# Kernel optimization log

Measured on AMD Instinct MI355X. Metric: run time of the kernel, lower is better.

Reference implementation:

```python
import jax, jax.numpy as jnp
import numpy as np

C = 1.0  # Poincare ball curvature
EPS = 1e-15


def setup_inputs() -> dict:
    key = jax.random.key(0)
    k1, k2, k3 = jax.random.split(key, 3)
    B, S, D_IN, D_OUT = 16, 8192, 128, 128
    # points strictly inside the unit ball: ||x|| ~ 0.05*sqrt(128) ~ 0.57
    x = 0.05 * jax.random.normal(k1, (B, S, D_IN), dtype=jnp.float32)
    z = 0.01 * jax.random.normal(k2, (D_IN, D_OUT), dtype=jnp.float32)  # init_std=0.01 normal
    r = 0.01 * jax.random.normal(k3, (D_OUT,), dtype=jnp.float32)
    return {"x": x, "z": z, "r": r}


def reference(x, z, r):
    # Poincare MLR (Shimizu et al., Hyperbolic NN++), as in hypll PoincareBall.mlr
    c = jnp.asarray(C, x.dtype)
    cs = jnp.sqrt(c)
    prefix = x.shape[:-1]
    x2 = x.reshape(-1, x.shape[-1])                       # [N, d_in]
    # conformal factor lambda_x = 2 / (1 - c ||x||^2)
    lam = 2.0 / (1.0 - c * jnp.sum(x2 * x2, axis=-1, keepdims=True))  # [N, 1]
    z_norm = jnp.maximum(jnp.linalg.norm(z, axis=0), EPS)             # [d_out]
    two_csr = 2.0 * cs * r                                            # [d_out]
    inner = x2 @ z                                                    # [N, d_out]
    arg = (cs * lam * inner / z_norm) * jnp.cosh(two_csr) - (lam - 1.0) * jnp.sinh(two_csr)
    out = (2.0 * z_norm / cs) * jnp.arcsinh(arg)                      # [N, d_out]
    return out.reshape(*prefix, z.shape[1])
```

## Files before the change

kernel.cpp:

```cpp
#include <hip/hip_runtime.h>
#include <cstdint>


typedef __attribute__((ext_vector_type(8))) short short8;
typedef __attribute__((ext_vector_type(4))) float floatx4;

#define D 128

__device__ inline unsigned bf16_rne(float f) {
    unsigned u = __float_as_uint(f);
    return ((u + 0x7FFFu + ((u >> 16) & 1u)) >> 16) & 0xFFFFu;
}

__global__ void hmlr_prep(const float* __restrict__ z, const float* __restrict__ r,
                          unsigned short* __restrict__ zt, float4* __restrict__ abs4) {
    int n = blockIdx.x;
    int k = threadIdx.x;
    float v = z[k * D + n];
    zt[n * D + k] = (unsigned short)bf16_rne(v);
    float p = v * v;
    #pragma unroll
    for (int off = 32; off >= 1; off >>= 1) p += __shfl_down(p, off, 64);
    __shared__ float tmp[2];
    if ((k & 63) == 0) tmp[k >> 6] = p;
    __syncthreads();
    if (k == 0) {
        float ss = tmp[0] + tmp[1];
        float zn = fmaxf(sqrtf(ss), 1e-15f);
        float tc = 2.0f * r[n];
        abs4[n] = make_float4(coshf(tc) / zn, sinhf(tc), 2.0f * zn, 0.0f);
    }
}

__global__ __launch_bounds__(512, 4) void hmlr_main(const float* __restrict__ x,
                                                    const unsigned short* __restrict__ zt,
                                                    const float4* __restrict__ abs4,
                                                    float* __restrict__ out) {
    __shared__ __align__(16) unsigned char lds[65536];
    #define LDS_Z 32768

    const int t    = threadIdx.x;
    const int w    = t >> 6;
    const int l    = t & 63;
    const int quad = l >> 4;
    const int l15  = l & 15;
    const int l7   = l15 & 7;

    const int rowbase = blockIdx.x * 128 + w * 16;

    const uint4* ztg = reinterpret_cast<const uint4*>(zt);
    uint4 zreg[4];
    #pragma unroll
    for (int i = 0; i < 4; ++i) zreg[i] = ztg[t + (i << 9)];

    const float4* xg = reinterpret_cast<const float4*>(x) + (size_t)blockIdx.x * 4096 + w * 512;
    float4 xv[8];
    #pragma unroll
    for (int j = 0; j < 8; ++j) xv[j] = xg[(j << 6) + l];

    float s[8];
    #pragma unroll
    for (int j = 0; j < 8; ++j) {
        float4 v = xv[j];
        int f   = (j << 6) + l;
        int row = w * 16 + (f >> 5);
        int fc  = f & 31;
        float p = v.x * v.x + v.y * v.y + v.z * v.z + v.w * v.w;
        p += __shfl_xor(p, 1);
        p += __shfl_xor(p, 2);
        p += __shfl_xor(p, 4);
        p += __shfl_xor(p, 8);
        p += __shfl_xor(p, 16);
        s[j] = p;
        unsigned lo = bf16_rne(v.x) | (bf16_rne(v.y) << 16);
        unsigned hi = bf16_rne(v.z) | (bf16_rne(v.w) << 16);
        int byte = (row << 8) + ((((fc >> 1) ^ (row & 7)) << 4)) + ((fc & 1) << 3);
        *reinterpret_cast<uint2*>(&lds[byte]) = make_uint2(lo, hi);
    }

    int idx3 = (l >> 1) & 7;
    float a0 = (idx3 & 1) ? s[1] : s[0];
    float a1 = (idx3 & 1) ? s[3] : s[2];
    float a2 = (idx3 & 1) ? s[5] : s[4];
    float a3 = (idx3 & 1) ? s[7] : s[6];
    float b0 = (idx3 & 2) ? a1 : a0;
    float b1 = (idx3 & 2) ? a3 : a2;
    float vsel = (idx3 & 4) ? b1 : b0;
    float usel = __shfl_xor(vsel, 32);
    float rq = (((l >> 5) & 1) == (l & 1)) ? vsel : usel;

    short8 afrag[4];
    #pragma unroll
    for (int kc = 0; kc < 4; ++kc) {
        int byte = ((w * 16 + l15) << 8) + (((quad + (kc << 2)) ^ l7) << 4);
        afrag[kc] = *reinterpret_cast<const short8*>(&lds[byte]);
    }

    #pragma unroll
    for (int i = 0; i < 4; ++i) {
        int idx = t + (i << 9);
        int row = idx >> 4, c = idx & 15;
        int byte = LDS_Z + (row << 8) + (((c ^ (row & 7)) << 4));
        *reinterpret_cast<uint4*>(&lds[byte]) = zreg[i];
    }
    __syncthreads();

    float4 cst[8];
    #pragma unroll
    for (int nt = 0; nt < 8; ++nt) cst[nt] = abs4[nt * 16 + l15];

    floatx4 acc[8];
    #pragma unroll
    for (int nt = 0; nt < 8; ++nt) acc[nt] = (floatx4){0.f, 0.f, 0.f, 0.f};

    #pragma unroll
    for (int kc = 0; kc < 4; ++kc) {
        #pragma unroll
        for (int nt = 0; nt < 8; ++nt) {
            int byte = LDS_Z + ((nt * 16 + l15) << 8) + (((quad + (kc << 2)) ^ l7) << 4);
            short8 b = *reinterpret_cast<const short8*>(&lds[byte]);
            acc[nt] = __builtin_amdgcn_mfma_f32_16x16x32_bf16(afrag[kc], b, acc[nt], 0, 0, 0);
        }
    }

    #pragma unroll
    for (int reg = 0; reg < 4; ++reg) {
        float rss = __shfl(rq, (quad << 2) | reg);
        float lam = 2.0f / (1.0f - rss);
        float lm1 = lam - 1.0f;
        float* orow = out + (size_t)(rowbase + (quad << 2) + reg) * D + l15;
        #pragma unroll
        for (int nt = 0; nt < 8; ++nt) {
            float inner = acc[nt][reg];
            float arg = __fmaf_rn(lam * inner, cst[nt].x, -lm1 * cst[nt].y);
            float a   = fabsf(arg);
            float as  = __logf(a + __fsqrt_rn(__fmaf_rn(a, a, 1.0f)));
            orow[nt * 16] = copysignf(as, arg) * cst[nt].z;
        }
    }
    #undef LDS_Z
}

extern "C" void kernel_launch(void* const* d_in, const int* in_sizes, int n_in,
                              void* d_out, int out_size, void* d_ws, size_t ws_size,
                              hipStream_t stream) {
    const float* x = (const float*)d_in[0];
    const float* z = (const float*)d_in[1];
    const float* r = (const float*)d_in[2];
    float* out = (float*)d_out;

    char* wsb = (char*)d_ws;
    unsigned short* zt = (unsigned short*)wsb;
    float4* abs4 = (float4*)(wsb + 128 * D * sizeof(unsigned short));

    hmlr_prep<<<128, 128, 0, stream>>>(z, r, zt, abs4);

    const int n_rows = in_sizes[0] / D;
    hmlr_main<<<n_rows / 128, 512, 0, stream>>>(x, zt, abs4, out);
}
```

Before: 125.4 us.

## Stage accumulators through LDS for float4 output stores, compute norms via MFMA

Computes the squared row norms with an extra MFMA of each A fragment against itself, taking the diagonal, in place of the shuffle reductions on the fp32 inputs. The epilogue writes accumulators into reused LDS in two passes and reads them back so each lane stores contiguous float4 rows, giving coalesced output writes. Per-column constants move to separate arrays loaded as float4. The norm is now taken from bf16-rounded inputs, which loses some precision, and the LDS round trip adds traffic and branching.

```diff
diff --git a/kernel.cpp b/kernel.cpp
--- a/kernel.cpp
+++ b/kernel.cpp
@@ -13,7 +13,8 @@
 }
 
 __global__ void hmlr_prep(const float* __restrict__ z, const float* __restrict__ r,
-                          unsigned short* __restrict__ zt, float4* __restrict__ abs4) {
+                          unsigned short* __restrict__ zt, float* __restrict__ An,
+                          float* __restrict__ Bn, float* __restrict__ Sn) {
     int n = blockIdx.x;
     int k = threadIdx.x;
     float v = z[k * D + n];
@@ -28,13 +29,17 @@
         float ss = tmp[0] + tmp[1];
         float zn = fmaxf(sqrtf(ss), 1e-15f);
         float tc = 2.0f * r[n];
-        abs4[n] = make_float4(coshf(tc) / zn, sinhf(tc), 2.0f * zn, 0.0f);
+        An[n] = coshf(tc) / zn;
+        Bn[n] = sinhf(tc);
+        Sn[n] = 2.0f * zn;
     }
 }
 
 __global__ __launch_bounds__(512, 4) void hmlr_main(const float* __restrict__ x,
                                                     const unsigned short* __restrict__ zt,
-                                                    const float4* __restrict__ abs4,
+                                                    const float* __restrict__ An,
+                                                    const float* __restrict__ Bn,
+                                                    const float* __restrict__ Sn,
                                                     float* __restrict__ out) {
     __shared__ __align__(16) unsigned char lds[65536];
     #define LDS_Z 32768
@@ -58,36 +63,17 @@
     #pragma unroll
     for (int j = 0; j < 8; ++j) xv[j] = xg[(j << 6) + l];
 
-    float s[8];
     #pragma unroll
     for (int j = 0; j < 8; ++j) {
         float4 v = xv[j];
         int f   = (j << 6) + l;
         int row = w * 16 + (f >> 5);
         int fc  = f & 31;
-        float p = v.x * v.x + v.y * v.y + v.z * v.z + v.w * v.w;
-        p += __shfl_xor(p, 1);
-        p += __shfl_xor(p, 2);
-        p += __shfl_xor(p, 4);
-        p += __shfl_xor(p, 8);
-        p += __shfl_xor(p, 16);
-        s[j] = p;
         unsigned lo = bf16_rne(v.x) | (bf16_rne(v.y) << 16);
         unsigned hi = bf16_rne(v.z) | (bf16_rne(v.w) << 16);
         int byte = (row << 8) + ((((fc >> 1) ^ (row & 7)) << 4)) + ((fc & 1) << 3);
         *reinterpret_cast<uint2*>(&lds[byte]) = make_uint2(lo, hi);
     }
-
-    int idx3 = (l >> 1) & 7;
-    float a0 = (idx3 & 1) ? s[1] : s[0];
-    float a1 = (idx3 & 1) ? s[3] : s[2];
-    float a2 = (idx3 & 1) ? s[5] : s[4];
-    float a3 = (idx3 & 1) ? s[7] : s[6];
-    float b0 = (idx3 & 2) ? a1 : a0;
-    float b1 = (idx3 & 2) ? a3 : a2;
-    float vsel = (idx3 & 4) ? b1 : b0;
-    float usel = __shfl_xor(vsel, 32);
-    float rq = (((l >> 5) & 1) == (l & 1)) ? vsel : usel;
 
     short8 afrag[4];
     #pragma unroll
@@ -105,16 +91,19 @@
     }
     __syncthreads();
 
-    float4 cst[8];
-    #pragma unroll
-    for (int nt = 0; nt < 8; ++nt) cst[nt] = abs4[nt * 16 + l15];
+    const int col0 = (l & 31) << 2;
+    float4 A4 = *reinterpret_cast<const float4*>(An + col0);
+    float4 B4 = *reinterpret_cast<const float4*>(Bn + col0);
+    float4 S4 = *reinterpret_cast<const float4*>(Sn + col0);
 
     floatx4 acc[8];
     #pragma unroll
     for (int nt = 0; nt < 8; ++nt) acc[nt] = (floatx4){0.f, 0.f, 0.f, 0.f};
+    floatx4 accd = (floatx4){0.f, 0.f, 0.f, 0.f};
 
     #pragma unroll
     for (int kc = 0; kc < 4; ++kc) {
+        accd = __builtin_amdgcn_mfma_f32_16x16x32_bf16(afrag[kc], afrag[kc], accd, 0, 0, 0);
         #pragma unroll
         for (int nt = 0; nt < 8; ++nt) {
             int byte = LDS_Z + ((nt * 16 + l15) << 8) + (((quad + (kc << 2)) ^ l7) << 4);
@@ -123,19 +112,54 @@
         }
     }
 
+    float cand = accd[l15 & 3];
+
+    float4* outv = reinterpret_cast<float4*>(out + (size_t)rowbase * D);
+    const int pbase = w << 12;
+
     #pragma unroll
-    for (int reg = 0; reg < 4; ++reg) {
-        float rss = __shfl(rq, (quad << 2) | reg);
-        float lam = 2.0f / (1.0f - rss);
-        float lm1 = lam - 1.0f;
-        float* orow = out + (size_t)(rowbase + (quad << 2) + reg) * D + l15;
+    for (int pass = 0; pass < 2; ++pass) {
+        if ((quad >> 1) == pass) {
+            int pr = (quad & 1) << 2;
+            #pragma unroll
+            for (int reg = 0; reg < 4; ++reg) {
+                #pragma unroll
+                for (int nt = 0; nt < 8; ++nt) {
+                    int byte = pbase + ((pr + reg) << 9) + ((l15 + (nt << 4)) << 2);
+                    *reinterpret_cast<float*>(&lds[byte]) = acc[nt][reg];
+                }
+            }
+        }
         #pragma unroll
-        for (int nt = 0; nt < 8; ++nt) {
-            float inner = acc[nt][reg];
-            float arg = __fmaf_rn(lam * inner, cst[nt].x, -lm1 * cst[nt].y);
-            float a   = fabsf(arg);
-            float as  = __logf(a + __fsqrt_rn(__fmaf_rn(a, a, 1.0f)));
-            orow[nt * 16] = copysignf(as, arg) * cst[nt].z;
+        for (int j = 0; j < 4; ++j) {
+            int fi = (j << 6) + l;
+            float4 v = *reinterpret_cast<const float4*>(&lds[pbase + (fi << 4)]);
+            int rl = (pass << 3) + (fi >> 5);
+            float ssq = __shfl(cand, ((rl >> 2) << 4) + rl);
+            float lam = 2.0f / (1.0f - ssq);
+            float lm1 = lam - 1.0f;
+            float4 res;
+            {
+                float arg = __fmaf_rn(lam * v.x, A4.x, -lm1 * B4.x);
+                float a = fabsf(arg);
+                res.x = copysignf(__logf(a + __fsqrt_rn(__fmaf_rn(a, a, 1.0f))), arg) * S4.x;
+            }
+            {
+                float arg = __fmaf_rn(lam * v.y, A4.y, -lm1 * B4.y);
+                float a = fabsf(arg);
+                res.y = copysignf(__logf(a + __fsqrt_rn(__fmaf_rn(a, a, 1.0f))), arg) * S4.y;
+            }
+            {
+                float arg = __fmaf_rn(lam * v.z, A4.z, -lm1 * B4.z);
+                float a = fabsf(arg);
+                res.z = copysignf(__logf(a + __fsqrt_rn(__fmaf_rn(a, a, 1.0f))), arg) * S4.z;
+            }
+            {
+                float arg = __fmaf_rn(lam * v.w, A4.w, -lm1 * B4.w);
+                float a = fabsf(arg);
+                res.w = copysignf(__logf(a + __fsqrt_rn(__fmaf_rn(a, a, 1.0f))), arg) * S4.w;
+            }
+            outv[(pass << 8) + fi] = res;
         }
     }
     #undef LDS_Z
@@ -151,10 +175,12 @@
 
     char* wsb = (char*)d_ws;
     unsigned short* zt = (unsigned short*)wsb;
-    float4* abs4 = (float4*)(wsb + 128 * D * sizeof(unsigned short));
+    float* An = (float*)(wsb + 128 * D * sizeof(unsigned short));
+    float* Bn = An + 128;
+    float* Sn = An + 256;
 
-    hmlr_prep<<<128, 128, 0, stream>>>(z, r, zt, abs4);
+    hmlr_prep<<<128, 128, 0, stream>>>(z, r, zt, An, Bn, Sn);
 
     const int n_rows = in_sizes[0] / D;
-    hmlr_main<<<n_rows / 128, 512, 0, stream>>>(x, zt, abs4, out);
+    hmlr_main<<<n_rows / 128, 512, 0, stream>>>(x, zt, An, Bn, Sn, out);
 }
```

New measurement: 124.0 us. Within noise of the previous version (-1.1%).
